# Performance work log

Measured on AMD Instinct MI355X. Metric: run time of the kernel, lower is better.

Reference implementation:

```python
import jax, jax.numpy as jnp
import numpy as np

B, N, DF, DC = 16, 4096, 128, 3
N_GROUP, K_GROUP = 1024, 16
D_IN, D_OUT = DC + DF, 256  # d_features = [131, 256]
BN_EPS = 1e-5


def farthest_point_sample(coord, n_sample):
    # coord: [B, N, 3] -> idx: [B, n_sample] (deterministic start at point 0)
    b, n, _ = coord.shape
    dist0 = jnp.full((b, n), jnp.inf, coord.dtype)
    idx0 = jnp.zeros((b,), jnp.int32)

    def step(carry, _):
        dist, last = carry
        last_pt = jnp.take_along_axis(coord, last[:, None, None].astype(jnp.int32), axis=1)  # [B,1,3]
        d = jnp.sum((coord - last_pt) ** 2, axis=-1)  # [B,N]
        dist = jnp.minimum(dist, d)
        nxt = jnp.argmax(dist, axis=1).astype(jnp.int32)
        return (dist, nxt), last

    _, idxs = jax.lax.scan(step, (dist0, idx0), None, length=n_sample)
    return jnp.swapaxes(idxs, 0, 1)  # [B, n_sample]


def knn_points(coord, center_coord, k):
    # squared distances [B, G, N]; k nearest source points per center
    d2 = jnp.sum((center_coord[:, :, None, :] - coord[:, None, :, :]) ** 2, axis=-1)
    _, idx = jax.lax.top_k(-d2, k)  # [B, G, k]
    return idx.astype(jnp.int32)


def index_points(points, idx):
    # points: [B, N, C]; idx: [B, ...] -> [B, ..., C]
    b = points.shape[0]
    batch_idx = jnp.arange(b).reshape((b,) + (1,) * (idx.ndim - 1))
    return points[batch_idx, idx]


def setup_inputs() -> dict:
    key = jax.random.key(0)
    k1, k2, k3, k4 = jax.random.split(key, 4)
    feature = jax.random.normal(k1, (B, N, DF), dtype=jnp.float32)
    coord = jax.random.normal(k2, (B, N, DC), dtype=jnp.float32)
    W = jax.random.normal(k3, (D_OUT, D_IN), dtype=jnp.float32) * (1.0 / np.sqrt(D_IN))
    b = jax.random.normal(k4, (D_OUT,), dtype=jnp.float32) * 0.01
    gamma = jnp.ones((D_OUT,), dtype=jnp.float32)
    beta = jnp.zeros((D_OUT,), dtype=jnp.float32)
    return {"feature": feature, "coord": coord, "W": W, "b": b, "gamma": gamma, "beta": beta}


def reference(feature, coord, W, b, gamma, beta):
    # --- group ---
    center_idx = farthest_point_sample(coord, N_GROUP)            # [B,G]
    center_coord = index_points(coord, center_idx)                 # [B,G,3]
    neigh_idx = knn_points(coord, center_coord, K_GROUP)           # [B,G,K]
    neigh_coord = index_points(coord, neigh_idx) - center_coord[:, :, None]  # [B,G,K,3]
    neigh_feature = jnp.concatenate([neigh_coord, index_points(feature, neigh_idx)], axis=-1)  # [B,G,K,131]
    # --- 1x1 conv + BatchNorm (train-mode batch stats, biased var) + ReLU ---
    y = jnp.einsum('bgkc,oc->bgko', neigh_feature, W) + b          # [B,G,K,256]
    mean = jnp.mean(y, axis=(0, 1, 2))
    var = jnp.mean((y - mean) ** 2, axis=(0, 1, 2))
    y = (y - mean) * jax.lax.rsqrt(var + BN_EPS) * gamma + beta
    y = jax.nn.relu(y)
    # --- max over neighbors ---
    center_feature = jnp.max(y, axis=2)                            # [B,G,256]
    return center_feature, center_coord
```

## Files before the change

kernel.cpp:

```cpp
#include <hip/hip_runtime.h>
#include <stdint.h>

#define BATCH 16
#define NPTS 4096
#define DFEAT 128
#define NGRP 1024
#define KNNK 16
#define DOUT_CH 256
#define KPAD 160
#define APAD 168
#define NGROUPS (BATCH*NGRP)
#define MROWS (NGROUPS*KNNK)
#define GEMM_BLOCKS (NGROUPS/8)
#define OUT_FEAT_ELEMS (NGROUPS*DOUT_CH)

typedef __attribute__((ext_vector_type(8))) short s16x8;
typedef __attribute__((ext_vector_type(8))) __bf16 bf16x8;
typedef __attribute__((ext_vector_type(4))) float f32x4;

union V8U { s16x8 s; bf16x8 b; };

__device__ inline unsigned short f2bf(float f) {
  unsigned u = __float_as_uint(f);
  unsigned r = 0x7FFFu + ((u >> 16) & 1u);
  return (unsigned short)((u + r) >> 16);
}

__device__ inline float sqdist3(float ax, float ay, float az,
                                float bx, float by, float bz) {
  float dx = __fsub_rn(ax, bx);
  float dy = __fsub_rn(ay, by);
  float dz = __fsub_rn(az, bz);
  return __fadd_rn(__fadd_rn(__fmul_rn(dx, dx), __fmul_rn(dy, dy)), __fmul_rn(dz, dz));
}

__device__ inline unsigned long long u64max(unsigned long long a, unsigned long long b) {
  return a > b ? a : b;
}

template<int CTRL>
__device__ inline unsigned long long dpp_max_step(unsigned long long k) {
  unsigned hi = (unsigned)(k >> 32), lo = (unsigned)k;
  unsigned hi2 = (unsigned)__builtin_amdgcn_update_dpp(0, (int)hi, CTRL, 0xF, 0xF, true);
  unsigned lo2 = (unsigned)__builtin_amdgcn_update_dpp(0, (int)lo, CTRL, 0xF, 0xF, true);
  unsigned long long k2 = ((unsigned long long)hi2 << 32) | lo2;
  return k2 > k ? k2 : k;
}

__device__ inline unsigned long long wave_max_u64(unsigned long long k) {
  k = dpp_max_step<0xB1>(k);
  k = dpp_max_step<0x4E>(k);
  k = dpp_max_step<0x141>(k);
  k = dpp_max_step<0x140>(k);
  k = dpp_max_step<0x142>(k);
  k = dpp_max_step<0x143>(k);
  return k;
}

__global__ __launch_bounds__(256)
void fps_wcast_kernel(const float* __restrict__ coord, const float* __restrict__ W,
                      float* __restrict__ out_coord, unsigned short* __restrict__ Wb)
{
  if (blockIdx.x >= BATCH) {
    for (int i = threadIdx.x; i < DOUT_CH * KPAD; i += 256) {
      int n = i / KPAD;
      int k = i - n * KPAD;
      float v = 0.f;
      if (k < 128)      v = W[n * 131 + 3 + k];
      else if (k < 131) v = W[n * 131 + (k - 128)];
      Wb[i] = f2bf(v);
    }
    return;
  }
  const int b = blockIdx.x;
  const int t = threadIdx.x;
  const int w = t >> 6;
  const int lane = t & 63;
  __shared__ float4 c4[NPTS];
  __shared__ float ocb[NGRP * 3];
  __shared__ unsigned long long slots[2][4];

  {
    const float* g = coord + (size_t)b * NPTS * 3;
    for (int p = t; p < NPTS; p += 256)
      c4[p] = make_float4(g[3 * p], g[3 * p + 1], g[3 * p + 2], 0.f);
  }
  __syncthreads();

  float px[16], py[16], pz[16], dist[16];
  unsigned lokey[16];
  #pragma unroll
  for (int j = 0; j < 16; ++j) {
    int p = t + 256 * j;
    float4 c = c4[p];
    px[j] = c.x; py[j] = c.y; pz[j] = c.z;
    dist[j] = __builtin_inff();
    lokey[j] = 0xFFFFFFFFu - (unsigned)p;
  }

  float lx = c4[0].x, ly = c4[0].y, lz = c4[0].z;
  if (t == 0) { ocb[0] = lx; ocb[1] = ly; ocb[2] = lz; }

  for (int i = 1; i < NGRP; ++i) {
    const int par = i & 1;

    unsigned long long cand[16];
    #pragma unroll
    for (int j = 0; j < 16; ++j) {
      float d  = sqdist3(px[j], py[j], pz[j], lx, ly, lz);
      float nd = fminf(dist[j], d);
      dist[j] = nd;
      cand[j] = ((unsigned long long)__float_as_uint(nd) << 32) | lokey[j];
    }
    #pragma unroll
    for (int st = 8; st >= 1; st >>= 1)
      #pragma unroll
      for (int j = 0; j < st; ++j)
        cand[j] = u64max(cand[j], cand[j + st]);
    unsigned long long best = cand[0];

    best = wave_max_u64(best);
    if (lane == 63) slots[par][w] = best;
    __syncthreads();

    unsigned long long s0 = u64max(slots[par][0], slots[par][1]);
    unsigned long long s1 = u64max(slots[par][2], slots[par][3]);
    unsigned long long f = u64max(s0, s1);
    int mi = (int)(0xFFFFFFFFu - (unsigned)(f & 0xFFFFFFFFull));

    float4 cw = c4[mi];
    lx = cw.x; ly = cw.y; lz = cw.z;
    if (t < 3) ocb[3 * i + t] = (t == 0) ? cw.x : ((t == 1) ? cw.y : cw.z);
  }

  __syncthreads();
  float* oc = out_coord + (size_t)b * NGRP * 3;
  #pragma unroll
  for (int qq = 0; qq < 12; ++qq) oc[t + 256 * qq] = ocb[t + 256 * qq];
}

#define KNN_SLOTS 512
__global__ __launch_bounds__(128)
void knn_kernel(const float* __restrict__ coord, const float* __restrict__ cent,
                int* __restrict__ nidx)
{
  __shared__ float sd[2 * NPTS];
  __shared__ float svd[2 * KNN_SLOTS];
  __shared__ int   svi[2 * KNN_SLOTS];

  const int w = threadIdx.x >> 6;
  const int lane = threadIdx.x & 63;
  const int c = blockIdx.x * 2 + w;
  const int b = c >> 10;
  float* wd  = sd  + w * NPTS;
  float* wsd = svd + w * KNN_SLOTS;
  int*   wsi = svi + w * KNN_SLOTS;

  const float cx = cent[c * 3], cy = cent[c * 3 + 1], cz = cent[c * 3 + 2];
  const float* pc = coord + (size_t)b * NPTS * 3;

  float m = __builtin_inff();
  for (int tt = 0; tt < 64; ++tt) {
    int p = tt * 64 + lane;
    float d = sqdist3(cx, cy, cz, pc[3 * p], pc[3 * p + 1], pc[3 * p + 2]);
    wd[p] = d;
    m = fminf(m, d);
  }
  unsigned mb = __float_as_uint(m);
  unsigned prefix = 0u;
  for (int bit = 30; bit >= 0; --bit) {
    unsigned trial = prefix | (1u << bit);
    unsigned long long ball = __ballot(mb < trial);
    if (__popcll(ball) < 16) prefix = trial;
  }
  const unsigned T = prefix;

  int base = 0;
  unsigned long long ltmask = (1ull << lane) - 1ull;
  for (int tt = 0; tt < 64; ++tt) {
    int p = tt * 64 + lane;
    float d = wd[p];
    bool keep = (__float_as_uint(d) <= T);
    unsigned long long mk = __ballot(keep);
    if (keep) {
      int pos = base + __popcll(mk & ltmask);
      if (pos < KNN_SLOTS) { wsd[pos] = d; wsi[pos] = p; }
    }
    base += __popcll(mk);
  }
  int S = base < KNN_SLOTS ? base : KNN_SLOTS;

  for (int r = 0; r < KNNK; ++r) {
    float bd = __builtin_inff(); int bs = 0x7fffffff;
    for (int s = lane; s < S; s += 64) {
      float d = wsd[s];
      if (d < bd) { bd = d; bs = s; }
    }
    #pragma unroll
    for (int off = 1; off < 64; off <<= 1) {
      float od = __shfl_xor(bd, off);
      int   os = __shfl_xor(bs, off);
      if (od < bd || (od == bd && os < bs)) { bd = od; bs = os; }
    }
    if (lane == 0) {
      nidx[c * KNNK + r] = wsi[bs];
      wsd[bs] = __builtin_inff();
    }
    __syncthreads();
  }
}

__global__ __launch_bounds__(256)
void gemm_kernel(const float* __restrict__ feat, const float* __restrict__ coord,
                 const float* __restrict__ cent, const int* __restrict__ nidx,
                 const unsigned short* __restrict__ Wb,
                 float* __restrict__ psum, float* __restrict__ psumsq,
                 float* __restrict__ wmax, float* __restrict__ wmin)
{
  __shared__ unsigned short Abuf[2][16][APAD];
  const int tid = threadIdx.x;
  const int w = tid >> 6, lane = tid & 63;
  const int lr = lane & 15, q = lane >> 4;
  const int g0 = blockIdx.x * 8;
  const int b = g0 >> 10;

  for (int i = tid; i < 2 * 16 * 32; i += 256) {
    int buf = i >> 9, rr = (i >> 5) & 15, cc = 128 + (i & 31);
    Abuf[buf][rr][cc] = 0;
  }

  V8U bfrag[4][5];
  #pragma unroll
  for (int nt = 0; nt < 4; ++nt)
    #pragma unroll
    for (int kt = 0; kt < 5; ++kt) {
      int n = w * 64 + nt * 16 + lr;
      bfrag[nt][kt].s = *(const s16x8*)(Wb + n * KPAD + kt * 32 + q * 8);
    }

  float sum1[4] = {0, 0, 0, 0}, sum2[4] = {0, 0, 0, 0};

  auto stage = [&](int gi, int buf) {
    int g = g0 + gi;
    int r = tid >> 4, c16 = tid & 15;
    int np = nidx[g * 16 + r];
    const float* fr = feat + ((size_t)(b * NPTS + np)) * DFEAT + c16 * 8;
    float4 f0 = ((const float4*)fr)[0];
    float4 f1 = ((const float4*)fr)[1];
    s16x8 v;
    v[0] = f2bf(f0.x); v[1] = f2bf(f0.y); v[2] = f2bf(f0.z); v[3] = f2bf(f0.w);
    v[4] = f2bf(f1.x); v[5] = f2bf(f1.y); v[6] = f2bf(f1.z); v[7] = f2bf(f1.w);
    *(s16x8*)&Abuf[buf][r][c16 * 8] = v;
    if (tid < 16) {
      int np2 = nidx[g * 16 + tid];
      const float* p = coord + ((size_t)(b * NPTS + np2)) * 3;
      float gx = cent[g * 3], gy = cent[g * 3 + 1], gz = cent[g * 3 + 2];
      Abuf[buf][tid][128] = f2bf(p[0] - gx);
      Abuf[buf][tid][129] = f2bf(p[1] - gy);
      Abuf[buf][tid][130] = f2bf(p[2] - gz);
    }
  };

  __syncthreads();
  stage(0, 0);
  __syncthreads();

  for (int gi = 0; gi < 8; ++gi) {
    int cur = gi & 1;
    if (gi < 7) stage(gi + 1, cur ^ 1);

    f32x4 acc[4];
    #pragma unroll
    for (int nt = 0; nt < 4; ++nt) acc[nt] = (f32x4)0.0f;
    #pragma unroll
    for (int kt = 0; kt < 5; ++kt) {
      V8U a;
      a.s = *(const s16x8*)&Abuf[cur][lr][kt * 32 + q * 8];
      #pragma unroll
      for (int nt = 0; nt < 4; ++nt)
        acc[nt] = __builtin_amdgcn_mfma_f32_16x16x32_bf16(a.b, bfrag[nt][kt].b, acc[nt], 0, 0, 0);
    }
    int g = g0 + gi;
    #pragma unroll
    for (int nt = 0; nt < 4; ++nt) {
      float r0 = acc[nt][0], r1 = acc[nt][1], r2 = acc[nt][2], r3 = acc[nt][3];
      float mx = fmaxf(fmaxf(r0, r1), fmaxf(r2, r3));
      float mn = fminf(fminf(r0, r1), fminf(r2, r3));
      sum1[nt] += r0 + r1 + r2 + r3;
      sum2[nt] += r0 * r0 + r1 * r1 + r2 * r2 + r3 * r3;
      mx = fmaxf(mx, __shfl_xor(mx, 16)); mn = fminf(mn, __shfl_xor(mn, 16));
      mx = fmaxf(mx, __shfl_xor(mx, 32)); mn = fminf(mn, __shfl_xor(mn, 32));
      if (q == 0) {
        int col = w * 64 + nt * 16 + lr;
        wmax[(size_t)g * DOUT_CH + col] = mx;
        wmin[(size_t)g * DOUT_CH + col] = mn;
      }
    }
    __syncthreads();
  }
  #pragma unroll
  for (int nt = 0; nt < 4; ++nt) {
    float s1 = sum1[nt], s2 = sum2[nt];
    s1 += __shfl_xor(s1, 16); s2 += __shfl_xor(s2, 16);
    s1 += __shfl_xor(s1, 32); s2 += __shfl_xor(s2, 32);
    if (q == 0) {
      int col = w * 64 + nt * 16 + lr;
      psum[(size_t)col * GEMM_BLOCKS + blockIdx.x]   = s1;
      psumsq[(size_t)col * GEMM_BLOCKS + blockIdx.x] = s2;
    }
  }
}

__global__ __launch_bounds__(256)
void stats_kernel(const float* __restrict__ psum, const float* __restrict__ psumsq,
                  const float* __restrict__ gamma, const float* __restrict__ beta,
                  float* __restrict__ sc, float* __restrict__ tc)
{
  const int c = blockIdx.x;
  const int tid = threadIdx.x, lane = tid & 63, w = tid >> 6;
  float s1 = 0.f, s2 = 0.f;
  for (int r = tid; r < GEMM_BLOCKS; r += 256) {
    s1 += psum[(size_t)c * GEMM_BLOCKS + r];
    s2 += psumsq[(size_t)c * GEMM_BLOCKS + r];
  }
  #pragma unroll
  for (int off = 1; off < 64; off <<= 1) { s1 += __shfl_xor(s1, off); s2 += __shfl_xor(s2, off); }
  __shared__ float a1[4], a2[4];
  if (lane == 0) { a1[w] = s1; a2[w] = s2; }
  __syncthreads();
  if (tid == 0) {
    float S1 = a1[0] + a1[1] + a1[2] + a1[3];
    float S2 = a2[0] + a2[1] + a2[2] + a2[3];
    const float inv = 1.0f / (float)MROWS;
    float mean = S1 * inv;
    float var  = S2 * inv - mean * mean;
    float rs = rsqrtf(var + 1e-5f);
    float s = gamma[c] * rs;
    sc[c] = s;
    tc[c] = beta[c] - mean * s;
  }
}

__global__ __launch_bounds__(256)
void final_kernel(const float* __restrict__ wmax, const float* __restrict__ wmin,
                  const float* __restrict__ sc, const float* __restrict__ tc,
                  float* __restrict__ out)
{
  int i4 = blockIdx.x * 256 + threadIdx.x;
  int base = i4 * 4;
  int c = base & (DOUT_CH - 1);
  float4 mx = *(const float4*)(wmax + base);
  float4 mn = *(const float4*)(wmin + base);
  float4 sv = *(const float4*)(sc + c);
  float4 tv = *(const float4*)(tc + c);
  float4 o;
  o.x = fmaxf(fmaf(sv.x, (sv.x > 0.f ? mx.x : mn.x), tv.x), 0.f);
  o.y = fmaxf(fmaf(sv.y, (sv.y > 0.f ? mx.y : mn.y), tv.y), 0.f);
  o.z = fmaxf(fmaf(sv.z, (sv.z > 0.f ? mx.z : mn.z), tv.z), 0.f);
  o.w = fmaxf(fmaf(sv.w, (sv.w > 0.f ? mx.w : mn.w), tv.w), 0.f);
  *(float4*)(out + base) = o;
}

extern "C" void kernel_launch(void* const* d_in, const int* in_sizes, int n_in,
                              void* d_out, int out_size, void* d_ws, size_t ws_size,
                              hipStream_t stream)
{
  const float* feature = (const float*)d_in[0];
  const float* coord   = (const float*)d_in[1];
  const float* W       = (const float*)d_in[2];
  const float* gamma   = (const float*)d_in[4];
  const float* beta    = (const float*)d_in[5];
  float* out = (float*)d_out;
  float* out_coord = out + OUT_FEAT_ELEMS;

  char* ws = (char*)d_ws;
  int*            nidx   = (int*)(ws + 0);
  unsigned short* Wb     = (unsigned short*)(ws + (1 << 20));
  float*          psum   = (float*)(ws + (2 << 20));
  float*          psumsq = (float*)(ws + (4 << 20));
  float*          sc     = (float*)(ws + (6 << 20));
  float*          tc     = (float*)(ws + (6 << 20) + 4096);
  float*          wmax   = (float*)(ws + (8 << 20));
  float*          wmin   = (float*)(ws + (8 << 20) + (size_t)OUT_FEAT_ELEMS * 4);

  hipLaunchKernelGGL(fps_wcast_kernel, dim3(BATCH + 1), dim3(256), 0, stream,
                     coord, W, out_coord, Wb);
  hipLaunchKernelGGL(knn_kernel, dim3(NGROUPS / 2), dim3(128), 0, stream,
                     coord, out_coord, nidx);
  hipLaunchKernelGGL(gemm_kernel, dim3(GEMM_BLOCKS), dim3(256), 0, stream,
                     feature, coord, out_coord, nidx, Wb, psum, psumsq, wmax, wmin);
  hipLaunchKernelGGL(stats_kernel, dim3(DOUT_CH), dim3(256), 0, stream,
                     psum, psumsq, gamma, beta, sc, tc);
  hipLaunchKernelGGL(final_kernel, dim3(OUT_FEAT_ELEMS / 1024), dim3(256), 0, stream,
                     wmax, wmin, sc, tc, out);
}
```

Baseline: 967.5 us.

## Fuse FPS, KNN and GEMM into one persistent kernel with progress flags

Merges the FPS, KNN and GEMM stages into a single persistent launch. Sixteen blocks run FPS and publish per-batch progress every eight centers through release atomics. 240 worker blocks spin on those flags so they can run KNN and GEMM for groups that are already available while FPS is still going. The change also swaps the serial KNN top-k selection for a register-resident DPP wave-min, and removes the global nidx round trip. In exchange it depends on all blocks being co-resident and on spin-waiting, which risks deadlock or contention, and the large shared-memory union may lower occupancy.

```diff
diff --git a/kernel.cpp b/kernel.cpp
--- a/kernel.cpp
+++ b/kernel.cpp
@@ -11,8 +11,11 @@
 #define APAD 168
 #define NGROUPS (BATCH*NGRP)
 #define MROWS (NGROUPS*KNNK)
-#define GEMM_BLOCKS (NGROUPS/8)
+#define NWORKERS 240
+#define NCHUNKS (NGROUPS/8)
+#define CHUNKS_PER_BATCH (NGRP/8)
 #define OUT_FEAT_ELEMS (NGROUPS*DOUT_CH)
+#define KNN_SLOTS 512
 
 typedef __attribute__((ext_vector_type(8))) short s16x8;
 typedef __attribute__((ext_vector_type(8))) __bf16 bf16x8;
@@ -46,7 +49,6 @@
   unsigned long long k2 = ((unsigned long long)hi2 << 32) | lo2;
   return k2 > k ? k2 : k;
 }
-
 __device__ inline unsigned long long wave_max_u64(unsigned long long k) {
   k = dpp_max_step<0xB1>(k);
   k = dpp_max_step<0x4E>(k);
@@ -57,12 +59,135 @@
   return k;
 }
 
+template<int CTRL>
+__device__ inline unsigned long long dpp_min_step(unsigned long long k) {
+  unsigned hi = (unsigned)(k >> 32), lo = (unsigned)k;
+  unsigned hi2 = (unsigned)__builtin_amdgcn_update_dpp((int)hi, (int)hi, CTRL, 0xF, 0xF, false);
+  unsigned lo2 = (unsigned)__builtin_amdgcn_update_dpp((int)lo, (int)lo, CTRL, 0xF, 0xF, false);
+  unsigned long long k2 = ((unsigned long long)hi2 << 32) | lo2;
+  return k2 < k ? k2 : k;
+}
+__device__ inline unsigned long long wave_min_u64(unsigned long long k) {
+  k = dpp_min_step<0xB1>(k);
+  k = dpp_min_step<0x4E>(k);
+  k = dpp_min_step<0x141>(k);
+  k = dpp_min_step<0x140>(k);
+  k = dpp_min_step<0x142>(k);
+  k = dpp_min_step<0x143>(k);
+  return k;
+}
+
+struct FpsSh {
+  float4 c4[NPTS];
+  float ocb[NGRP * 3];
+  unsigned long long slots[2][4];
+};
+struct WrkSh {
+  float wd[4][NPTS];
+  float svd[4][KNN_SLOTS];
+  int   svi[4][KNN_SLOTS];
+  unsigned short Abuf[2][16][APAD];
+  int   nidx_s[8][KNNK];
+  float cent_s[8][3];
+};
+union ShU { FpsSh f; WrkSh w; };
+
 __global__ __launch_bounds__(256)
-void fps_wcast_kernel(const float* __restrict__ coord, const float* __restrict__ W,
-                      float* __restrict__ out_coord, unsigned short* __restrict__ Wb)
+void fused_kernel(const float* __restrict__ feat, const float* __restrict__ coord,
+                  const float* __restrict__ W, float* __restrict__ out_coord,
+                  unsigned short* __restrict__ Wb,
+                  float* __restrict__ psum, float* __restrict__ psumsq,
+                  float* __restrict__ wmax, float* __restrict__ wmin,
+                  int* __restrict__ progress, int* __restrict__ wb_ready)
 {
-  if (blockIdx.x >= BATCH) {
-    for (int i = threadIdx.x; i < DOUT_CH * KPAD; i += 256) {
+  __shared__ ShU sh;
+  const int tid = threadIdx.x;
+  const int w = tid >> 6;
+  const int lane = tid & 63;
+
+  if (blockIdx.x < BATCH) {
+    const int b = blockIdx.x;
+    float4* c4 = sh.f.c4;
+    float* ocb = sh.f.ocb;
+
+    const float* g = coord + (size_t)b * NPTS * 3;
+    for (int p = tid; p < NPTS; p += 256)
+      c4[p] = make_float4(g[3 * p], g[3 * p + 1], g[3 * p + 2], 0.f);
+    __syncthreads();
+
+    float px[16], py[16], pz[16], dist[16];
+    unsigned lokey[16];
+    #pragma unroll
+    for (int j = 0; j < 16; ++j) {
+      int p = tid + 256 * j;
+      float4 c = c4[p];
+      px[j] = c.x; py[j] = c.y; pz[j] = c.z;
+      dist[j] = __builtin_inff();
+      lokey[j] = 0xFFFFFFFFu - (unsigned)p;
+    }
+
+    float lx = c4[0].x, ly = c4[0].y, lz = c4[0].z;
+    if (tid == 0) { ocb[0] = lx; ocb[1] = ly; ocb[2] = lz; }
+
+    float* oc = out_coord + (size_t)b * NGRP * 3;
+    int pend = 0;
+
+    for (int i = 1; i < NGRP; ++i) {
+      const int par = i & 1;
+      unsigned long long cand[16];
+      #pragma unroll
+      for (int j = 0; j < 16; ++j) {
+        float d  = sqdist3(px[j], py[j], pz[j], lx, ly, lz);
+        float nd = fminf(dist[j], d);
+        dist[j] = nd;
+        cand[j] = ((unsigned long long)__float_as_uint(nd) << 32) | lokey[j];
+      }
+      #pragma unroll
+      for (int st = 8; st >= 1; st >>= 1)
+        #pragma unroll
+        for (int j = 0; j < st; ++j)
+          cand[j] = u64max(cand[j], cand[j + st]);
+      unsigned long long best = wave_max_u64(cand[0]);
+      if (lane == 63) sh.f.slots[par][w] = best;
+      __syncthreads();
+
+      if (pend) {
+        if (tid == 0) {
+          __threadfence();
+          __hip_atomic_store(&progress[b], pend, __ATOMIC_RELEASE, __HIP_MEMORY_SCOPE_AGENT);
+        }
+        pend = 0;
+      }
+      if ((i & 7) == 0) {
+        if (tid < 24) oc[(i - 8) * 3 + tid] = ocb[(i - 8) * 3 + tid];
+        pend = i;
+      }
+
+      unsigned long long s0 = u64max(sh.f.slots[par][0], sh.f.slots[par][1]);
+      unsigned long long s1 = u64max(sh.f.slots[par][2], sh.f.slots[par][3]);
+      unsigned long long f = u64max(s0, s1);
+      int mi = (int)(0xFFFFFFFFu - (unsigned)(f & 0xFFFFFFFFull));
+
+      float4 cw = c4[mi];
+      lx = cw.x; ly = cw.y; lz = cw.z;
+      if (tid < 3) ocb[3 * i + tid] = (tid == 0) ? cw.x : ((tid == 1) ? cw.y : cw.z);
+    }
+
+    __syncthreads();
+    #pragma unroll
+    for (int qq = 0; qq < 12; ++qq) oc[tid + 256 * qq] = ocb[tid + 256 * qq];
+    __syncthreads();
+    if (tid == 0) {
+      __threadfence();
+      __hip_atomic_store(&progress[b], NGRP, __ATOMIC_RELEASE, __HIP_MEMORY_SCOPE_AGENT);
+    }
+    return;
+  }
+
+  const int wi = blockIdx.x - BATCH;
+
+  if (wi == 0) {
+    for (int i = tid; i < DOUT_CH * KPAD; i += 256) {
       int n = i / KPAD;
       int k = i - n * KPAD;
       float v = 0.f;
@@ -70,164 +195,20 @@
       else if (k < 131) v = W[n * 131 + (k - 128)];
       Wb[i] = f2bf(v);
     }
-    return;
-  }
-  const int b = blockIdx.x;
-  const int t = threadIdx.x;
-  const int w = t >> 6;
-  const int lane = t & 63;
-  __shared__ float4 c4[NPTS];
-  __shared__ float ocb[NGRP * 3];
-  __shared__ unsigned long long slots[2][4];
-
-  {
-    const float* g = coord + (size_t)b * NPTS * 3;
-    for (int p = t; p < NPTS; p += 256)
-      c4[p] = make_float4(g[3 * p], g[3 * p + 1], g[3 * p + 2], 0.f);
+    __syncthreads();
+    if (tid == 0) {
+      __threadfence();
+      __hip_atomic_store(wb_ready, 1, __ATOMIC_RELEASE, __HIP_MEMORY_SCOPE_AGENT);
+    }
+  }
+  if (tid == 0) {
+    while (__hip_atomic_load(wb_ready, __ATOMIC_RELAXED, __HIP_MEMORY_SCOPE_AGENT) == 0)
+      __builtin_amdgcn_s_sleep(1);
+    __threadfence();
   }
   __syncthreads();
 
-  float px[16], py[16], pz[16], dist[16];
-  unsigned lokey[16];
-  #pragma unroll
-  for (int j = 0; j < 16; ++j) {
-    int p = t + 256 * j;
-    float4 c = c4[p];
-    px[j] = c.x; py[j] = c.y; pz[j] = c.z;
-    dist[j] = __builtin_inff();
-    lokey[j] = 0xFFFFFFFFu - (unsigned)p;
-  }
-
-  float lx = c4[0].x, ly = c4[0].y, lz = c4[0].z;
-  if (t == 0) { ocb[0] = lx; ocb[1] = ly; ocb[2] = lz; }
-
-  for (int i = 1; i < NGRP; ++i) {
-    const int par = i & 1;
-
-    unsigned long long cand[16];
-    #pragma unroll
-    for (int j = 0; j < 16; ++j) {
-      float d  = sqdist3(px[j], py[j], pz[j], lx, ly, lz);
-      float nd = fminf(dist[j], d);
-      dist[j] = nd;
-      cand[j] = ((unsigned long long)__float_as_uint(nd) << 32) | lokey[j];
-    }
-    #pragma unroll
-    for (int st = 8; st >= 1; st >>= 1)
-      #pragma unroll
-      for (int j = 0; j < st; ++j)
-        cand[j] = u64max(cand[j], cand[j + st]);
-    unsigned long long best = cand[0];
-
-    best = wave_max_u64(best);
-    if (lane == 63) slots[par][w] = best;
-    __syncthreads();
-
-    unsigned long long s0 = u64max(slots[par][0], slots[par][1]);
-    unsigned long long s1 = u64max(slots[par][2], slots[par][3]);
-    unsigned long long f = u64max(s0, s1);
-    int mi = (int)(0xFFFFFFFFu - (unsigned)(f & 0xFFFFFFFFull));
-
-    float4 cw = c4[mi];
-    lx = cw.x; ly = cw.y; lz = cw.z;
-    if (t < 3) ocb[3 * i + t] = (t == 0) ? cw.x : ((t == 1) ? cw.y : cw.z);
-  }
-
-  __syncthreads();
-  float* oc = out_coord + (size_t)b * NGRP * 3;
-  #pragma unroll
-  for (int qq = 0; qq < 12; ++qq) oc[t + 256 * qq] = ocb[t + 256 * qq];
-}
-
-#define KNN_SLOTS 512
-__global__ __launch_bounds__(128)
-void knn_kernel(const float* __restrict__ coord, const float* __restrict__ cent,
-                int* __restrict__ nidx)
-{
-  __shared__ float sd[2 * NPTS];
-  __shared__ float svd[2 * KNN_SLOTS];
-  __shared__ int   svi[2 * KNN_SLOTS];
-
-  const int w = threadIdx.x >> 6;
-  const int lane = threadIdx.x & 63;
-  const int c = blockIdx.x * 2 + w;
-  const int b = c >> 10;
-  float* wd  = sd  + w * NPTS;
-  float* wsd = svd + w * KNN_SLOTS;
-  int*   wsi = svi + w * KNN_SLOTS;
-
-  const float cx = cent[c * 3], cy = cent[c * 3 + 1], cz = cent[c * 3 + 2];
-  const float* pc = coord + (size_t)b * NPTS * 3;
-
-  float m = __builtin_inff();
-  for (int tt = 0; tt < 64; ++tt) {
-    int p = tt * 64 + lane;
-    float d = sqdist3(cx, cy, cz, pc[3 * p], pc[3 * p + 1], pc[3 * p + 2]);
-    wd[p] = d;
-    m = fminf(m, d);
-  }
-  unsigned mb = __float_as_uint(m);
-  unsigned prefix = 0u;
-  for (int bit = 30; bit >= 0; --bit) {
-    unsigned trial = prefix | (1u << bit);
-    unsigned long long ball = __ballot(mb < trial);
-    if (__popcll(ball) < 16) prefix = trial;
-  }
-  const unsigned T = prefix;
-
-  int base = 0;
-  unsigned long long ltmask = (1ull << lane) - 1ull;
-  for (int tt = 0; tt < 64; ++tt) {
-    int p = tt * 64 + lane;
-    float d = wd[p];
-    bool keep = (__float_as_uint(d) <= T);
-    unsigned long long mk = __ballot(keep);
-    if (keep) {
-      int pos = base + __popcll(mk & ltmask);
-      if (pos < KNN_SLOTS) { wsd[pos] = d; wsi[pos] = p; }
-    }
-    base += __popcll(mk);
-  }
-  int S = base < KNN_SLOTS ? base : KNN_SLOTS;
-
-  for (int r = 0; r < KNNK; ++r) {
-    float bd = __builtin_inff(); int bs = 0x7fffffff;
-    for (int s = lane; s < S; s += 64) {
-      float d = wsd[s];
-      if (d < bd) { bd = d; bs = s; }
-    }
-    #pragma unroll
-    for (int off = 1; off < 64; off <<= 1) {
-      float od = __shfl_xor(bd, off);
-      int   os = __shfl_xor(bs, off);
-      if (od < bd || (od == bd && os < bs)) { bd = od; bs = os; }
-    }
-    if (lane == 0) {
-      nidx[c * KNNK + r] = wsi[bs];
-      wsd[bs] = __builtin_inff();
-    }
-    __syncthreads();
-  }
-}
-
-__global__ __launch_bounds__(256)
-void gemm_kernel(const float* __restrict__ feat, const float* __restrict__ coord,
-                 const float* __restrict__ cent, const int* __restrict__ nidx,
-                 const unsigned short* __restrict__ Wb,
-                 float* __restrict__ psum, float* __restrict__ psumsq,
-                 float* __restrict__ wmax, float* __restrict__ wmin)
-{
-  __shared__ unsigned short Abuf[2][16][APAD];
-  const int tid = threadIdx.x;
-  const int w = tid >> 6, lane = tid & 63;
   const int lr = lane & 15, q = lane >> 4;
-  const int g0 = blockIdx.x * 8;
-  const int b = g0 >> 10;
-
-  for (int i = tid; i < 2 * 16 * 32; i += 256) {
-    int buf = i >> 9, rr = (i >> 5) & 15, cc = 128 + (i & 31);
-    Abuf[buf][rr][cc] = 0;
-  }
 
   V8U bfrag[4][5];
   #pragma unroll
@@ -238,66 +219,148 @@
       bfrag[nt][kt].s = *(const s16x8*)(Wb + n * KPAD + kt * 32 + q * 8);
     }
 
+  for (int i = tid; i < 2 * 16 * 32; i += 256) {
+    int buf = i >> 9, rr = (i >> 5) & 15, cc = 128 + (i & 31);
+    sh.w.Abuf[buf][rr][cc] = 0;
+  }
   float sum1[4] = {0, 0, 0, 0}, sum2[4] = {0, 0, 0, 0};
-
-  auto stage = [&](int gi, int buf) {
-    int g = g0 + gi;
-    int r = tid >> 4, c16 = tid & 15;
-    int np = nidx[g * 16 + r];
-    const float* fr = feat + ((size_t)(b * NPTS + np)) * DFEAT + c16 * 8;
-    float4 f0 = ((const float4*)fr)[0];
-    float4 f1 = ((const float4*)fr)[1];
-    s16x8 v;
-    v[0] = f2bf(f0.x); v[1] = f2bf(f0.y); v[2] = f2bf(f0.z); v[3] = f2bf(f0.w);
-    v[4] = f2bf(f1.x); v[5] = f2bf(f1.y); v[6] = f2bf(f1.z); v[7] = f2bf(f1.w);
-    *(s16x8*)&Abuf[buf][r][c16 * 8] = v;
-    if (tid < 16) {
-      int np2 = nidx[g * 16 + tid];
-      const float* p = coord + ((size_t)(b * NPTS + np2)) * 3;
-      float gx = cent[g * 3], gy = cent[g * 3 + 1], gz = cent[g * 3 + 2];
-      Abuf[buf][tid][128] = f2bf(p[0] - gx);
-      Abuf[buf][tid][129] = f2bf(p[1] - gy);
-      Abuf[buf][tid][130] = f2bf(p[2] - gz);
-    }
-  };
-
   __syncthreads();
-  stage(0, 0);
-  __syncthreads();
-
-  for (int gi = 0; gi < 8; ++gi) {
-    int cur = gi & 1;
-    if (gi < 7) stage(gi + 1, cur ^ 1);
-
-    f32x4 acc[4];
-    #pragma unroll
-    for (int nt = 0; nt < 4; ++nt) acc[nt] = (f32x4)0.0f;
-    #pragma unroll
-    for (int kt = 0; kt < 5; ++kt) {
-      V8U a;
-      a.s = *(const s16x8*)&Abuf[cur][lr][kt * 32 + q * 8];
-      #pragma unroll
-      for (int nt = 0; nt < 4; ++nt)
-        acc[nt] = __builtin_amdgcn_mfma_f32_16x16x32_bf16(a.b, bfrag[nt][kt].b, acc[nt], 0, 0, 0);
-    }
-    int g = g0 + gi;
-    #pragma unroll
-    for (int nt = 0; nt < 4; ++nt) {
-      float r0 = acc[nt][0], r1 = acc[nt][1], r2 = acc[nt][2], r3 = acc[nt][3];
-      float mx = fmaxf(fmaxf(r0, r1), fmaxf(r2, r3));
-      float mn = fminf(fminf(r0, r1), fminf(r2, r3));
-      sum1[nt] += r0 + r1 + r2 + r3;
-      sum2[nt] += r0 * r0 + r1 * r1 + r2 * r2 + r3 * r3;
-      mx = fmaxf(mx, __shfl_xor(mx, 16)); mn = fminf(mn, __shfl_xor(mn, 16));
-      mx = fmaxf(mx, __shfl_xor(mx, 32)); mn = fminf(mn, __shfl_xor(mn, 32));
-      if (q == 0) {
-        int col = w * 64 + nt * 16 + lr;
-        wmax[(size_t)g * DOUT_CH + col] = mx;
-        wmin[(size_t)g * DOUT_CH + col] = mn;
-      }
-    }
-    __syncthreads();
-  }
+
+  for (int c = wi; c < NCHUNKS; c += NWORKERS) {
+    const int b = c >> 7;
+    const int lc = c & (CHUNKS_PER_BATCH - 1);
+    const int need = lc * 8 + 8;
+
+    if (tid == 0) {
+      while (__hip_atomic_load(&progress[b], __ATOMIC_RELAXED, __HIP_MEMORY_SCOPE_AGENT) < need)
+        __builtin_amdgcn_s_sleep(8);
+      __threadfence();
+    }
+    __syncthreads();
+
+    if (tid < 24) sh.w.cent_s[tid / 3][tid % 3] =
+        out_coord[(size_t)b * NGRP * 3 + lc * 24 + tid];
+    __syncthreads();
+
+    const float* pc = coord + (size_t)b * NPTS * 3;
+    for (int k2 = 0; k2 < 2; ++k2) {
+      const int k8 = w * 2 + k2;
+      const float cx = sh.w.cent_s[k8][0], cy = sh.w.cent_s[k8][1], cz = sh.w.cent_s[k8][2];
+      float* wd  = sh.w.wd[w];
+      float* wsd = sh.w.svd[w];
+      int*   wsi = sh.w.svi[w];
+
+      float m = __builtin_inff();
+      for (int tt = 0; tt < 64; ++tt) {
+        int p = tt * 64 + lane;
+        float d = sqdist3(cx, cy, cz, pc[3 * p], pc[3 * p + 1], pc[3 * p + 2]);
+        wd[p] = d;
+        m = fminf(m, d);
+      }
+      unsigned mb = __float_as_uint(m);
+      unsigned prefix = 0u;
+      for (int bit = 30; bit >= 0; --bit) {
+        unsigned trial = prefix | (1u << bit);
+        if (__popcll(__ballot(mb < trial)) < 16) prefix = trial;
+      }
+      const unsigned T = prefix;
+
+      int base = 0;
+      unsigned long long ltmask = (1ull << lane) - 1ull;
+      for (int tt = 0; tt < 64; ++tt) {
+        int p = tt * 64 + lane;
+        float d = wd[p];
+        bool keep = (__float_as_uint(d) <= T);
+        unsigned long long mk = __ballot(keep);
+        if (keep) {
+          int pos = base + __popcll(mk & ltmask);
+          if (pos < KNN_SLOTS) { wsd[pos] = d; wsi[pos] = p; }
+        }
+        base += __popcll(mk);
+      }
+      int S = base < KNN_SLOTS ? base : KNN_SLOTS;
+
+      float rsd[8];
+      #pragma unroll
+      for (int k = 0; k < 8; ++k) {
+        int s = lane + 64 * k;
+        rsd[k] = (s < S) ? wsd[s] : __builtin_inff();
+      }
+      for (int r = 0; r < KNNK; ++r) {
+        unsigned long long key = 0xFFFFFFFFFFFFFFFFull;
+        #pragma unroll
+        for (int k = 0; k < 8; ++k) {
+          unsigned long long kk = ((unsigned long long)__float_as_uint(rsd[k]) << 32)
+                                | (unsigned)(lane + 64 * k);
+          key = kk < key ? kk : key;
+        }
+        key = wave_min_u64(key);
+        int bs = __builtin_amdgcn_readlane((int)(unsigned)(key & 0xFFFFFFFFull), 63);
+        #pragma unroll
+        for (int k = 0; k < 8; ++k)
+          if (lane == (bs & 63) && k == (bs >> 6)) rsd[k] = __builtin_inff();
+        if (lane == 0) sh.w.nidx_s[k8][r] = wsi[bs];
+      }
+    }
+    __syncthreads();
+
+    auto stage = [&](int gi, int buf) {
+      int r = tid >> 4, c16 = tid & 15;
+      int np = sh.w.nidx_s[gi][r];
+      const float* fr = feat + ((size_t)(b * NPTS + np)) * DFEAT + c16 * 8;
+      float4 f0 = ((const float4*)fr)[0];
+      float4 f1 = ((const float4*)fr)[1];
+      s16x8 v;
+      v[0] = f2bf(f0.x); v[1] = f2bf(f0.y); v[2] = f2bf(f0.z); v[3] = f2bf(f0.w);
+      v[4] = f2bf(f1.x); v[5] = f2bf(f1.y); v[6] = f2bf(f1.z); v[7] = f2bf(f1.w);
+      *(s16x8*)&sh.w.Abuf[buf][r][c16 * 8] = v;
+      if (tid < 16) {
+        int np2 = sh.w.nidx_s[gi][tid];
+        const float* p = coord + ((size_t)(b * NPTS + np2)) * 3;
+        sh.w.Abuf[buf][tid][128] = f2bf(p[0] - sh.w.cent_s[gi][0]);
+        sh.w.Abuf[buf][tid][129] = f2bf(p[1] - sh.w.cent_s[gi][1]);
+        sh.w.Abuf[buf][tid][130] = f2bf(p[2] - sh.w.cent_s[gi][2]);
+      }
+    };
+
+    stage(0, 0);
+    __syncthreads();
+
+    for (int gi = 0; gi < 8; ++gi) {
+      int cur = gi & 1;
+      if (gi < 7) stage(gi + 1, cur ^ 1);
+
+      f32x4 acc[4];
+      #pragma unroll
+      for (int nt = 0; nt < 4; ++nt) acc[nt] = (f32x4)0.0f;
+      #pragma unroll
+      for (int kt = 0; kt < 5; ++kt) {
+        V8U a;
+        a.s = *(const s16x8*)&sh.w.Abuf[cur][lr][kt * 32 + q * 8];
+        #pragma unroll
+        for (int nt = 0; nt < 4; ++nt)
+          acc[nt] = __builtin_amdgcn_mfma_f32_16x16x32_bf16(a.b, bfrag[nt][kt].b, acc[nt], 0, 0, 0);
+      }
+      int gidx = c * 8 + gi;
+      #pragma unroll
+      for (int nt = 0; nt < 4; ++nt) {
+        float r0 = acc[nt][0], r1 = acc[nt][1], r2 = acc[nt][2], r3 = acc[nt][3];
+        float mx = fmaxf(fmaxf(r0, r1), fmaxf(r2, r3));
+        float mn = fminf(fminf(r0, r1), fminf(r2, r3));
+        sum1[nt] += r0 + r1 + r2 + r3;
+        sum2[nt] += r0 * r0 + r1 * r1 + r2 * r2 + r3 * r3;
+        mx = fmaxf(mx, __shfl_xor(mx, 16)); mn = fminf(mn, __shfl_xor(mn, 16));
+        mx = fmaxf(mx, __shfl_xor(mx, 32)); mn = fminf(mn, __shfl_xor(mn, 32));
+        if (q == 0) {
+          int col = w * 64 + nt * 16 + lr;
+          wmax[(size_t)gidx * DOUT_CH + col] = mx;
+          wmin[(size_t)gidx * DOUT_CH + col] = mn;
+        }
+      }
+      __syncthreads();
+    }
+  }
+
   #pragma unroll
   for (int nt = 0; nt < 4; ++nt) {
     float s1 = sum1[nt], s2 = sum2[nt];
@@ -305,8 +368,8 @@
     s1 += __shfl_xor(s1, 32); s2 += __shfl_xor(s2, 32);
     if (q == 0) {
       int col = w * 64 + nt * 16 + lr;
-      psum[(size_t)col * GEMM_BLOCKS + blockIdx.x]   = s1;
-      psumsq[(size_t)col * GEMM_BLOCKS + blockIdx.x] = s2;
+      psum[(size_t)col * NWORKERS + wi]   = s1;
+      psumsq[(size_t)col * NWORKERS + wi] = s2;
     }
   }
 }
@@ -319,9 +382,9 @@
   const int c = blockIdx.x;
   const int tid = threadIdx.x, lane = tid & 63, w = tid >> 6;
   float s1 = 0.f, s2 = 0.f;
-  for (int r = tid; r < GEMM_BLOCKS; r += 256) {
-    s1 += psum[(size_t)c * GEMM_BLOCKS + r];
-    s2 += psumsq[(size_t)c * GEMM_BLOCKS + r];
+  for (int r = tid; r < NWORKERS; r += 256) {
+    s1 += psum[(size_t)c * NWORKERS + r];
+    s2 += psumsq[(size_t)c * NWORKERS + r];
   }
   #pragma unroll
   for (int off = 1; off < 64; off <<= 1) { s1 += __shfl_xor(s1, off); s2 += __shfl_xor(s2, off); }
@@ -374,21 +437,22 @@
   float* out_coord = out + OUT_FEAT_ELEMS;
 
   char* ws = (char*)d_ws;
-  int*            nidx   = (int*)(ws + 0);
-  unsigned short* Wb     = (unsigned short*)(ws + (1 << 20));
-  float*          psum   = (float*)(ws + (2 << 20));
-  float*          psumsq = (float*)(ws + (4 << 20));
-  float*          sc     = (float*)(ws + (6 << 20));
-  float*          tc     = (float*)(ws + (6 << 20) + 4096);
+  int*            flags  = (int*)(ws + 0);
+  unsigned short* Wb     = (unsigned short*)(ws + 4096);
+  float*          psum   = (float*)(ws + (1 << 20));
+  float*          psumsq = (float*)(ws + (2 << 20));
+  float*          sc     = (float*)(ws + (3 << 20));
+  float*          tc     = (float*)(ws + (3 << 20) + 4096);
   float*          wmax   = (float*)(ws + (8 << 20));
   float*          wmin   = (float*)(ws + (8 << 20) + (size_t)OUT_FEAT_ELEMS * 4);
-
-  hipLaunchKernelGGL(fps_wcast_kernel, dim3(BATCH + 1), dim3(256), 0, stream,
-                     coord, W, out_coord, Wb);
-  hipLaunchKernelGGL(knn_kernel, dim3(NGROUPS / 2), dim3(128), 0, stream,
-                     coord, out_coord, nidx);
-  hipLaunchKernelGGL(gemm_kernel, dim3(GEMM_BLOCKS), dim3(256), 0, stream,
-                     feature, coord, out_coord, nidx, Wb, psum, psumsq, wmax, wmin);
+  int* progress = flags;
+  int* wb_ready = flags + 16;
+
+  hipMemsetAsync(flags, 0, 128, stream);
+
+  hipLaunchKernelGGL(fused_kernel, dim3(BATCH + NWORKERS), dim3(256), 0, stream,
+                     feature, coord, W, out_coord, Wb,
+                     psum, psumsq, wmax, wmin, progress, wb_ready);
   hipLaunchKernelGGL(stats_kernel, dim3(DOUT_CH), dim3(256), 0, stream,
                      psum, psumsq, gamma, beta, sc, tc);
   hipLaunchKernelGGL(final_kernel, dim3(OUT_FEAT_ELEMS / 1024), dim3(256), 0, stream,
```

New measurement: 1.101 ms. 1.14x slower.
